# Kernel optimization log

Measured on AMD Instinct MI355X. Metric: run time of the kernel, lower is better.

## Reference

```python
import jax, jax.numpy as jnp
import numpy as np

N_NODE = 2048   # n_node
N_TIME = 10     # t / look_back
STEP_K = 5
PROB_C = 0.98
LN_EPS = 1e-5


def setup_inputs() -> dict:
    key = jax.random.key(0)
    k1, k2 = jax.random.split(key, 2)
    # dynamic adjacency-like input: [n_node, n_time, n_node], nonnegative
    x = jax.random.uniform(k1, (N_NODE, N_TIME, N_NODE), dtype=jnp.float32)
    # learned restart weights, init = prob_c (already in [0,1])
    weight = jnp.full((N_TIME, STEP_K), PROB_C, dtype=jnp.float32)
    # LayerNorm(n_node) params
    ln_gamma = jnp.ones((N_NODE,), dtype=jnp.float32)
    ln_beta = jnp.zeros((N_NODE,), dtype=jnp.float32)
    return {"x": x, "weight": weight, "ln_gamma": ln_gamma, "ln_beta": ln_beta}


def _layer_norm(h, gamma, beta):
    mu = jnp.mean(h, axis=-1, keepdims=True)
    var = jnp.mean((h - mu) ** 2, axis=-1, keepdims=True)
    return (h - mu) * jax.lax.rsqrt(var + LN_EPS) * gamma + beta


def reference(x, weight, ln_gamma, ln_beta):
    # x: [N, T, N]; weight: [T, K]
    w = jnp.clip(weight, 0.0, 1.0)
    n = x.shape[0]
    eye = jnp.eye(n, dtype=x.dtype)  # Pt0

    G = jnp.transpose(x, (1, 0, 2))                 # [T, N, N]
    deg = jnp.sum(G, axis=-1, keepdims=True) + 1e-8  # row degree
    G_norm = G / deg                                # D^{-1} G (row-normalize)

    def per_time(Gt_norm, wt):
        # random walk with restart, accumulate sum of P over K steps
        def step(carry, wi):
            P, acc = carry
            Pc = wi * (P @ Gt_norm) + (1.0 - wi) * eye
            return (Pc, acc + Pc), None
        (_, final_P), _ = jax.lax.scan(step, (eye, jnp.zeros_like(eye)), wt)
        return _layer_norm(final_P, ln_gamma, ln_beta)

    out = jax.vmap(per_time)(G_norm, w)  # [T, N, N]
    return jnp.transpose(out, (1, 0, 2))  # [N, T, N]
```

## Files before the change

kernel.cpp:

```cpp
#include <hip/hip_runtime.h>
#include <stdint.h>

#define NN 2048
#define TT 10
#define KST 5
#define BK 64
#define NKT2 (NN / BK)

typedef float f32x4 __attribute__((ext_vector_type(4)));
typedef __bf16 bf16x8 __attribute__((ext_vector_type(8)));
typedef unsigned short u16x8 __attribute__((ext_vector_type(8)));

using as3_void = __attribute__((address_space(3))) void;
using as1_const_void = const __attribute__((address_space(1))) void;

__device__ __forceinline__ unsigned short f2bf_bits(float f) {
    unsigned u = __builtin_bit_cast(unsigned, f);
    unsigned r = u + 0x7FFFu + ((u >> 16) & 1u);
    return (unsigned short)(r >> 16);
}
__device__ __forceinline__ float bf2f(unsigned short b) {
    return __builtin_bit_cast(float, ((unsigned)b) << 16);
}

__global__ __launch_bounds__(256) void deg_kernel(const float* __restrict__ x,
                                                  float* __restrict__ deg) {
    const int i = blockIdx.x;
    const int t = blockIdx.y;
    const int tid = threadIdx.x;
    const float4* r4 = (const float4*)(x + ((size_t)i * TT + t) * NN);
    float4 a = r4[tid];
    float4 b = r4[tid + 256];
    float s = a.x + a.y + a.z + a.w + b.x + b.y + b.z + b.w;
    #pragma unroll
    for (int m = 32; m >= 1; m >>= 1) s += __shfl_xor(s, m, 64);
    __shared__ float red[4];
    if ((tid & 63) == 0) red[tid >> 6] = s;
    __syncthreads();
    if (tid == 0) deg[(size_t)t * NN + i] = red[0] + red[1] + red[2] + red[3] + 1e-8f;
}

__global__ __launch_bounds__(256) void gnt_init_kernel(const float* __restrict__ x,
                                                       const float* __restrict__ deg,
                                                       const float* __restrict__ w,
                                                       unsigned short* __restrict__ gnt,
                                                       unsigned short* __restrict__ p1,
                                                       int t0) {
    const int tl = blockIdx.z;
    const int t  = t0 + tl;
    float w0 = w[t * KST + 0];
    w0 = fminf(fmaxf(w0, 0.0f), 1.0f);
    const float om = 1.0f - w0;
    const int n0 = blockIdx.x * 64;
    const int k0 = blockIdx.y * 64;
    __shared__ float tile[64][65];
    const int tx = threadIdx.x & 63;
    const int ty = threadIdx.x >> 6;
    unsigned short* p1dst = p1 + (size_t)tl * NN * NN;
    #pragma unroll
    for (int p = 0; p < 16; ++p) {
        int kr = p * 4 + ty;
        float rd = 1.0f / deg[(size_t)t * NN + k0 + kr];
        float v = x[(((size_t)(k0 + kr)) * TT + t) * NN + n0 + tx] * rd;
        tile[kr][tx] = v;
        float pv = w0 * v + ((k0 + kr) == (n0 + tx) ? om : 0.0f);
        p1dst[(size_t)(k0 + kr) * NN + n0 + tx] = f2bf_bits(pv);
    }
    __syncthreads();
    unsigned short* dst = gnt + (size_t)tl * NN * NN;
    #pragma unroll
    for (int p = 0; p < 16; ++p) {
        int nr = p * 4 + ty;
        dst[(size_t)(n0 + nr) * NN + k0 + tx] = f2bf_bits(tile[tx][nr]);
    }
}

#define FENCE __asm__ volatile("" ::: "memory")

#define MFMA_PHASE(PA, PB, BARR)                                                  \
  do {                                                                            \
    _Pragma("unroll")                                                             \
    for (int f_ = 0; f_ < 4; ++f_) {                                              \
      _Pragma("unroll")                                                           \
      for (int g_ = 0; g_ < 2; ++g_) {                                            \
        acc[(PA)*4 + f_][(PB)*2 + g_] = __builtin_amdgcn_mfma_f32_16x16x32_bf16(  \
            af[f_][0], BARR[g_][0], acc[(PA)*4 + f_][(PB)*2 + g_], 0, 0, 0);      \
        acc[(PA)*4 + f_][(PB)*2 + g_] = __builtin_amdgcn_mfma_f32_16x16x32_bf16(  \
            af[f_][1], BARR[g_][1], acc[(PA)*4 + f_][(PB)*2 + g_], 0, 0, 0);      \
      }                                                                           \
    }                                                                             \
  } while (0)

__global__ __launch_bounds__(512, 2) void gemm_step256(
        const unsigned short* __restrict__ Pprev,
        const unsigned short* __restrict__ gnt,
        const float* __restrict__ w,
        unsigned short* __restrict__ Pnext,
        int t0, int kstep) {
    extern __shared__ char smem[];

    const int nwg  = (int)gridDim.x;
    const int flat = (int)blockIdx.x;
    const int xcd  = flat & 7;
    const int q    = nwg >> 3, r = nwg & 7;
    const int wgid = (xcd < r ? xcd * (q + 1) : r * (q + 1) + (xcd - r) * q) + (flat >> 3);
    const int tl   = wgid >> 6;
    const int s    = wgid & 63;
    const int g4   = s >> 2, w4 = s & 3;
    const int tm   = ((g4 >> 2) << 1) | (w4 >> 1);
    const int tn   = ((g4 & 3) << 1) | (w4 & 1);
    const int t    = t0 + tl;

    const int tid  = threadIdx.x;
    const int lane = tid & 63;
    const int wv   = tid >> 6;
    const int wm   = wv >> 2;
    const int wn   = wv & 3;
    const int lr   = lane & 15;
    const int quad = lane >> 4;
    const int swz  = lr & 7;

    const unsigned short* Ab = Pprev + (size_t)tl * NN * NN;
    const unsigned short* Bb = gnt   + (size_t)tl * NN * NN;

    const int srow  = lane >> 3;
    const int sslot = (lane & 7) ^ srow;
    const unsigned short* pa[2][2];
    const unsigned short* pb[2][2];
    #pragma unroll
    for (int h = 0; h < 2; ++h)
        #pragma unroll
        for (int l = 0; l < 2; ++l) {
            const int rA = tm * 256 + h * 128 + l * 64 + wv * 8 + srow;
            const int rB = tn * 256 + h * 128 + l * 64 + wv * 8 + srow;
            pa[h][l] = Ab + (size_t)rA * NN + sslot * 8;
            pb[h][l] = Bb + (size_t)rB * NN + sslot * 8;
        }

    auto stageA = [&](int kt, int b, int h) {
        #pragma unroll
        for (int l = 0; l < 2; ++l)
            __builtin_amdgcn_global_load_lds(
                (as1_const_void*)(pa[h][l] + kt * BK),
                (as3_void*)(smem + b * 65536 + h * 16384 + l * 8192 + wv * 1024),
                16, 0, 0);
    };
    auto stageB = [&](int kt, int b, int h) {
        #pragma unroll
        for (int l = 0; l < 2; ++l)
            __builtin_amdgcn_global_load_lds(
                (as1_const_void*)(pb[h][l] + kt * BK),
                (as3_void*)(smem + b * 65536 + 32768 + h * 16384 + l * 8192 + wv * 1024),
                16, 0, 0);
    };

    bf16x8 af[4][2];
    bf16x8 bf0[2][2];
    bf16x8 bf1[2][2];
    const int sA = ((quad)     ^ swz) * 16;
    const int sB = ((quad + 4) ^ swz) * 16;
    auto lda = [&](int b, int half) {
        const char* base = smem + b * 65536 + half * 16384 + (wm * 64 + lr) * 128;
        #pragma unroll
        for (int f = 0; f < 4; ++f) {
            af[f][0] = *(const bf16x8*)(base + f * 2048 + sA);
            af[f][1] = *(const bf16x8*)(base + f * 2048 + sB);
        }
    };
    auto ldb = [&](int b, int half, bf16x8 (&dst)[2][2]) {
        const char* base = smem + b * 65536 + 32768 + half * 16384 + (wn * 32 + lr) * 128;
        #pragma unroll
        for (int g = 0; g < 2; ++g) {
            dst[g][0] = *(const bf16x8*)(base + g * 2048 + sA);
            dst[g][1] = *(const bf16x8*)(base + g * 2048 + sB);
        }
    };

    f32x4 acc[8][4];
    #pragma unroll
    for (int i = 0; i < 8; ++i)
        #pragma unroll
        for (int j = 0; j < 4; ++j)
            acc[i][j] = (f32x4){0.0f, 0.0f, 0.0f, 0.0f};

    stageA(0, 0, 0);
    stageB(0, 0, 0);
    stageB(0, 0, 1);
    stageA(0, 0, 1);

    for (int kt = 0; kt < NKT2 - 1; ++kt) {
        const int buf  = kt & 1;
        const int nbuf = buf ^ 1;
        FENCE; __builtin_amdgcn_s_waitcnt(0xF74); __builtin_amdgcn_s_barrier(); FENCE;
        lda(buf, 0);
        ldb(buf, 0, bf0);
        stageA(kt + 1, nbuf, 0);
        stageB(kt + 1, nbuf, 0);
        __builtin_amdgcn_s_setprio(1);
        MFMA_PHASE(0, 0, bf0);
        __builtin_amdgcn_s_setprio(0);
        FENCE; __builtin_amdgcn_s_barrier(); FENCE;
        FENCE; __builtin_amdgcn_s_waitcnt(0xF76); __builtin_amdgcn_s_barrier(); FENCE;
        ldb(buf, 1, bf1);
        stageB(kt + 1, nbuf, 1);
        __builtin_amdgcn_s_setprio(1);
        MFMA_PHASE(0, 1, bf1);
        __builtin_amdgcn_s_setprio(0);
        FENCE; __builtin_amdgcn_s_barrier(); FENCE;
        FENCE; __builtin_amdgcn_s_waitcnt(0xF76); __builtin_amdgcn_s_barrier(); FENCE;
        lda(buf, 1);
        stageA(kt + 1, nbuf, 1);
        __builtin_amdgcn_s_setprio(1);
        MFMA_PHASE(1, 1, bf1);
        __builtin_amdgcn_s_setprio(0);
        FENCE; __builtin_amdgcn_s_barrier(); FENCE;
        __builtin_amdgcn_s_barrier(); FENCE;
        __builtin_amdgcn_s_setprio(1);
        MFMA_PHASE(1, 0, bf0);
        __builtin_amdgcn_s_setprio(0);
        FENCE; __builtin_amdgcn_s_barrier(); FENCE;
    }

    {
        const int buf = (NKT2 - 1) & 1;
        FENCE; __builtin_amdgcn_s_waitcnt(0xF74); __builtin_amdgcn_s_barrier(); FENCE;
        lda(buf, 0);
        ldb(buf, 0, bf0);
        __builtin_amdgcn_s_setprio(1);
        MFMA_PHASE(0, 0, bf0);
        __builtin_amdgcn_s_setprio(0);
        FENCE; __builtin_amdgcn_s_waitcnt(0xF72); __builtin_amdgcn_s_barrier(); FENCE;
        ldb(buf, 1, bf1);
        __builtin_amdgcn_s_setprio(1);
        MFMA_PHASE(0, 1, bf1);
        __builtin_amdgcn_s_setprio(0);
        FENCE; __builtin_amdgcn_s_waitcnt(0xF70); __builtin_amdgcn_s_barrier(); FENCE;
        lda(buf, 1);
        __builtin_amdgcn_s_setprio(1);
        MFMA_PHASE(1, 1, bf1);
        MFMA_PHASE(1, 0, bf0);
        __builtin_amdgcn_s_setprio(0);
    }

    float wk = w[t * KST + kstep];
    wk = fminf(fmaxf(wk, 0.0f), 1.0f);
    const float om = 1.0f - wk;
    unsigned short* __restrict__ Pn = Pnext + (size_t)tl * NN * NN;
    #pragma unroll
    for (int F = 0; F < 8; ++F) {
        const int mrow0 = tm * 256 + (F >> 2) * 128 + wm * 64 + (F & 3) * 16 + quad * 4;
        #pragma unroll
        for (int v = 0; v < 4; ++v) {
            const int m = mrow0 + v;
            const size_t mb = (size_t)m * NN;
            #pragma unroll
            for (int G = 0; G < 4; ++G) {
                const int n = tn * 256 + (G >> 1) * 128 + wn * 32 + (G & 1) * 16 + lr;
                float val = wk * acc[F][G][v] + (m == n ? om : 0.0f);
                Pn[mb + n] = f2bf_bits(val);
            }
        }
    }
}

__global__ __launch_bounds__(256) void ln_kernel(const unsigned short* __restrict__ Pall,
                                                 const float* __restrict__ gamma,
                                                 const float* __restrict__ beta,
                                                 float* __restrict__ out,
                                                 int t0, size_t strideK) {
    const int m  = blockIdx.x;
    const int tl = blockIdx.y;
    const int t  = t0 + tl;
    const int tid = threadIdx.x;
    const int j = tid * 8;

    const size_t rbase = (size_t)tl * NN * NN + (size_t)m * NN + j;
    float v[8] = {0, 0, 0, 0, 0, 0, 0, 0};
    #pragma unroll
    for (int k = 0; k < KST; ++k) {
        u16x8 pv = *(const u16x8*)(Pall + (size_t)k * strideK + rbase);
        #pragma unroll
        for (int e = 0; e < 8; ++e) v[e] += bf2f(pv[e]);
    }

    float s = 0.0f;
    #pragma unroll
    for (int e = 0; e < 8; ++e) s += v[e];
    #pragma unroll
    for (int mm = 32; mm >= 1; mm >>= 1) s += __shfl_xor(s, mm, 64);
    __shared__ float red[4];
    if ((tid & 63) == 0) red[tid >> 6] = s;
    __syncthreads();
    const float mu = (red[0] + red[1] + red[2] + red[3]) * (1.0f / NN);

    float q = 0.0f;
    float dx[8];
    #pragma unroll
    for (int e = 0; e < 8; ++e) { dx[e] = v[e] - mu; q += dx[e] * dx[e]; }
    __syncthreads();
    #pragma unroll
    for (int mm = 32; mm >= 1; mm >>= 1) q += __shfl_xor(q, mm, 64);
    if ((tid & 63) == 0) red[tid >> 6] = q;
    __syncthreads();
    const float var = (red[0] + red[1] + red[2] + red[3]) * (1.0f / NN);
    const float sc = rsqrtf(var + 1e-5f);

    float4 g0 = *(const float4*)(gamma + j);
    float4 g1 = *(const float4*)(gamma + j + 4);
    float4 b0 = *(const float4*)(beta + j);
    float4 b1 = *(const float4*)(beta + j + 4);
    const size_t ob = ((size_t)m * TT + t) * NN + j;
    float4 o0, o1;
    o0.x = dx[0] * sc * g0.x + b0.x;  o0.y = dx[1] * sc * g0.y + b0.y;
    o0.z = dx[2] * sc * g0.z + b0.z;  o0.w = dx[3] * sc * g0.w + b0.w;
    o1.x = dx[4] * sc * g1.x + b1.x;  o1.y = dx[5] * sc * g1.y + b1.y;
    o1.z = dx[6] * sc * g1.z + b1.z;  o1.w = dx[7] * sc * g1.w + b1.w;
    *(float4*)(out + ob)     = o0;
    *(float4*)(out + ob + 4) = o1;
}

extern "C" void kernel_launch(void* const* d_in, const int* in_sizes, int n_in,
                              void* d_out, int out_size, void* d_ws, size_t ws_size,
                              hipStream_t stream) {
    (void)in_sizes; (void)n_in; (void)out_size;
    const float* x     = (const float*)d_in[0];
    const float* w     = (const float*)d_in[1];
    const float* gamma = (const float*)d_in[2];
    const float* beta  = (const float*)d_in[3];
    float* out = (float*)d_out;

    static bool attr_done = false;
    if (!attr_done) {
        (void)hipFuncSetAttribute((const void*)gemm_step256,
                                  hipFuncAttributeMaxDynamicSharedMemorySize, 131072);
        attr_done = true;
    }

    char* ws = (char*)d_ws;
    float* deg = (float*)ws;
    size_t off = ((size_t)TT * NN * sizeof(float) + 255) & ~(size_t)255;
    const size_t per_t = (size_t)NN * NN * sizeof(unsigned short);
    size_t avail = ws_size > off ? ws_size - off : 0;
    int TB = (int)(avail / ((1 + KST) * per_t));
    if (TB < 1) TB = 1;
    if (TB > TT) TB = TT;
    unsigned short* gnt  = (unsigned short*)(ws + off);
    unsigned short* Pall = gnt + (size_t)TB * NN * NN;
    const size_t strideK = (size_t)TB * NN * NN;

    deg_kernel<<<dim3(NN, TT), 256, 0, stream>>>(x, deg);

    for (int t0 = 0; t0 < TT; t0 += TB) {
        const int tb = (TT - t0) < TB ? (TT - t0) : TB;
        gnt_init_kernel<<<dim3(32, 32, tb), 256, 0, stream>>>(x, deg, w, gnt, Pall, t0);
        for (int k = 2; k <= KST; ++k) {
            const unsigned short* Pp = Pall + (size_t)(k - 2) * strideK;
            unsigned short*       Pn = Pall + (size_t)(k - 1) * strideK;
            gemm_step256<<<dim3(64 * tb), 512, 131072, stream>>>(Pp, gnt, w, Pn, t0, k - 1);
        }
        ln_kernel<<<dim3(NN, tb), 256, 0, stream>>>(Pall, gamma, beta, out, t0, strideK);
    }
}
```

Baseline: 1.051 ms.

## Deepen GEMM prefetch pipeline to stage tiles two iterations ahead

Restructures the main K loop of the step GEMM so global-to-LDS staging of half-tiles runs up to two k-iterations ahead, reusing freed halves of the current buffer instead of strictly double-buffering one step ahead. The separate epilogue iteration is folded into the loop by clamping prefetch indices at the end, which adds redundant loads for the last tiles. Explicit lgkmcnt(0) waits with sched barriers replace some vmcnt waits before each MFMA phase. The aim is to hide more global-load latency behind MFMA work. The cost is tighter buffer-reuse ordering and extra barriers per iteration.

```diff
diff --git a/kernel.cpp b/kernel.cpp
--- a/kernel.cpp
+++ b/kernel.cpp
@@ -76,6 +76,8 @@
 }
 
 #define FENCE __asm__ volatile("" ::: "memory")
+#define LGKM0 do { __asm__ volatile("s_waitcnt lgkmcnt(0)" ::: "memory"); \
+                   __builtin_amdgcn_sched_barrier(0); } while (0)
 
 #define MFMA_PHASE(PA, PB, BARR)                                                  \
   do {                                                                            \
@@ -187,59 +189,47 @@
     stageB(0, 0, 0);
     stageB(0, 0, 1);
     stageA(0, 0, 1);
-
-    for (int kt = 0; kt < NKT2 - 1; ++kt) {
-        const int buf  = kt & 1;
-        const int nbuf = buf ^ 1;
-        FENCE; __builtin_amdgcn_s_waitcnt(0xF74); __builtin_amdgcn_s_barrier(); FENCE;
-        lda(buf, 0);
-        ldb(buf, 0, bf0);
-        stageA(kt + 1, nbuf, 0);
-        stageB(kt + 1, nbuf, 0);
+    stageA(1, 1, 0);
+    stageB(1, 1, 0);
+    stageB(1, 1, 1);
+    FENCE; __builtin_amdgcn_s_waitcnt(0xF76); __builtin_amdgcn_s_barrier(); FENCE;
+
+    for (int kt = 0; kt < NKT2; ++kt) {
+        const int b  = kt & 1;
+        const int nb = b ^ 1;
+        const int k1 = (kt + 1 < NKT2) ? kt + 1 : NKT2 - 1;
+        const int k2 = (kt + 2 < NKT2) ? kt + 2 : NKT2 - 1;
+
+        lda(b, 0);
+        ldb(b, 0, bf0);
+        stageA(k1, nb, 1);
+        FENCE; __builtin_amdgcn_s_barrier(); LGKM0;
         __builtin_amdgcn_s_setprio(1);
         MFMA_PHASE(0, 0, bf0);
         __builtin_amdgcn_s_setprio(0);
         FENCE; __builtin_amdgcn_s_barrier(); FENCE;
-        FENCE; __builtin_amdgcn_s_waitcnt(0xF76); __builtin_amdgcn_s_barrier(); FENCE;
-        ldb(buf, 1, bf1);
-        stageB(kt + 1, nbuf, 1);
+
+        ldb(b, 1, bf1);
+        stageA(k2, b, 0);
+        FENCE; __builtin_amdgcn_s_barrier(); LGKM0;
         __builtin_amdgcn_s_setprio(1);
         MFMA_PHASE(0, 1, bf1);
         __builtin_amdgcn_s_setprio(0);
         FENCE; __builtin_amdgcn_s_barrier(); FENCE;
-        FENCE; __builtin_amdgcn_s_waitcnt(0xF76); __builtin_amdgcn_s_barrier(); FENCE;
-        lda(buf, 1);
-        stageA(kt + 1, nbuf, 1);
+
+        lda(b, 1);
+        stageB(k2, b, 0);
+        FENCE; __builtin_amdgcn_s_barrier(); LGKM0;
         __builtin_amdgcn_s_setprio(1);
         MFMA_PHASE(1, 1, bf1);
         __builtin_amdgcn_s_setprio(0);
         FENCE; __builtin_amdgcn_s_barrier(); FENCE;
-        __builtin_amdgcn_s_barrier(); FENCE;
+
+        stageB(k2, b, 1);
         __builtin_amdgcn_s_setprio(1);
         MFMA_PHASE(1, 0, bf0);
         __builtin_amdgcn_s_setprio(0);
-        FENCE; __builtin_amdgcn_s_barrier(); FENCE;
-    }
-
-    {
-        const int buf = (NKT2 - 1) & 1;
-        FENCE; __builtin_amdgcn_s_waitcnt(0xF74); __builtin_amdgcn_s_barrier(); FENCE;
-        lda(buf, 0);
-        ldb(buf, 0, bf0);
-        __builtin_amdgcn_s_setprio(1);
-        MFMA_PHASE(0, 0, bf0);
-        __builtin_amdgcn_s_setprio(0);
-        FENCE; __builtin_amdgcn_s_waitcnt(0xF72); __builtin_amdgcn_s_barrier(); FENCE;
-        ldb(buf, 1, bf1);
-        __builtin_amdgcn_s_setprio(1);
-        MFMA_PHASE(0, 1, bf1);
-        __builtin_amdgcn_s_setprio(0);
-        FENCE; __builtin_amdgcn_s_waitcnt(0xF70); __builtin_amdgcn_s_barrier(); FENCE;
-        lda(buf, 1);
-        __builtin_amdgcn_s_setprio(1);
-        MFMA_PHASE(1, 1, bf1);
-        MFMA_PHASE(1, 0, bf0);
-        __builtin_amdgcn_s_setprio(0);
+        FENCE; __builtin_amdgcn_s_waitcnt(0xF76); __builtin_amdgcn_s_barrier(); FENCE;
     }
 
     float wk = w[t * KST + kstep];
```

Measured after the change: 1.091 ms. 1.04x slower.
